# Kernel tuning notes

Hardware: AMD Instinct MI355X
Metric: run time of the kernel (lower is better)

## Reference

```python
import jax, jax.numpy as jnp
import numpy as np

DN = ('NCHW', 'OIHW', 'NCHW')


def conv2d(x, w, b, stride):
    y = jax.lax.conv_general_dilated(x, w, (stride, stride), 'VALID', dimension_numbers=DN)
    return y + b[None, :, None, None]


def split_heads(t, heads):
    # 'B (c h) H W -> B h (H W) c'  (channel index = c*heads + h)
    B, C, H, W = t.shape
    c = C // heads
    t = t.reshape(B, c, heads, H * W)
    return jnp.transpose(t, (0, 2, 3, 1))  # [B, h, HW, c]


def setup_inputs() -> dict:
    key = jax.random.key(0)
    ks = jax.random.split(key, 7)
    B, dim, H, W = 4, 256, 128, 128
    inner, p = 256, 8
    s = 0.02
    return {
        'x':  jax.random.normal(ks[0], (B, dim, H, W), jnp.float32),
        'Wq': jax.random.normal(ks[1], (inner, dim, 1, 1), jnp.float32) * s,
        'bq': jax.random.normal(ks[2], (inner,), jnp.float32) * s,
        'Wk': jax.random.normal(ks[3], (inner, dim, p, p), jnp.float32) * s,
        'bk': jax.random.normal(ks[4], (inner,), jnp.float32) * s,
        'Wv': jax.random.normal(ks[5], (inner, dim, p, p), jnp.float32) * s,
        'bv': jax.random.normal(ks[6], (inner,), jnp.float32) * s,
    }


def reference(x, Wq, bq, Wk, bk, Wv, bv):
    heads = 8
    p = Wk.shape[-1]
    B, C, H, W = x.shape
    q = conv2d(x, Wq, bq, 1)      # [B, inner, H, W]
    k = conv2d(x, Wk, bk, p)      # [B, inner, H/p, W/p]
    v = conv2d(x, Wv, bv, p)
    q = split_heads(q, heads)     # [B, h, HW, c]
    k = split_heads(k, heads)     # [B, h, K, c]
    v = split_heads(v, heads)
    # NOTE: original module applies no 1/sqrt(d) scaling
    dots = jnp.einsum('bhnc,bhkc->bhnk', q, k)
    attn = jax.nn.softmax(dots, axis=-1)
    out = jnp.einsum('bhnk,bhkc->bhnc', attn, v)  # [B, h, HW, c]
    # 'B h (H W) c -> B (c h) H W'
    c = out.shape[-1]
    out = jnp.transpose(out, (0, 3, 1, 2)).reshape(B, c * heads, H, W)
    return out
```

## Files before the change

### kernel.cpp

```cpp
#include <hip/hip_runtime.h>
#include <stdint.h>

typedef short sh4 __attribute__((ext_vector_type(4)));
typedef short short8 __attribute__((ext_vector_type(8)));
typedef float f32x4 __attribute__((ext_vector_type(4)));
typedef _Float16 half4 __attribute__((ext_vector_type(4)));
typedef _Float16 half8 __attribute__((ext_vector_type(8)));
typedef unsigned int uint2v __attribute__((ext_vector_type(2)));

__device__ __forceinline__ short f2h(float f) {
    _Float16 h = (_Float16)f;
    return __builtin_bit_cast(short, h);
}

__device__ __forceinline__ f32x4 mfma_k32(short8 a, short8 b, f32x4 c) {
    return __builtin_amdgcn_mfma_f32_16x16x32_f16(
        __builtin_bit_cast(half8, a), __builtin_bit_cast(half8, b), c, 0, 0, 0);
}
__device__ __forceinline__ f32x4 mfma_k16(half4 a, half4 b, f32x4 c) {
    return __builtin_amdgcn_mfma_f32_16x16x16f16(a, b, c, 0, 0, 0);
}
__device__ __forceinline__ unsigned int pkrtz(float a, float b) {
    return __builtin_bit_cast(unsigned int, __builtin_amdgcn_cvt_pkrtz(a, b));
}
__device__ __forceinline__ float exp2_raw(float x) {
    float r;
    asm("v_exp_f32 %0, %1" : "=v"(r) : "v"(x));
    return r;
}


__device__ __forceinline__ void transpose64(const float* __restrict__ src,
                                            short* __restrict__ dst,
                                            int srcSlowStride, int dstRowStride) {
    __shared__ float tile[64][65];
    const int t = threadIdx.x;
#pragma unroll
    for (int i = 0; i < 16; ++i) {
        int idx = i * 256 + t;
        int fast = idx & 63, slow = idx >> 6;
        tile[slow][fast] = src[(long)slow * srcSlowStride + fast];
    }
    __syncthreads();
#pragma unroll
    for (int i = 0; i < 2; ++i) {
        int ch = i * 256 + t;
        int fast = ch >> 3, sg = ch & 7;
        short8 v;
#pragma unroll
        for (int j = 0; j < 8; ++j) v[j] = f2h(tile[sg * 8 + j][fast]);
        *(short8*)(dst + (long)fast * dstRowStride + sg * 8) = v;
    }
}

__global__ __launch_bounds__(256) void k_pack_x(const float* __restrict__ x,
                                                short* __restrict__ xn) {
    int bi = blockIdx.x;
    int ct = bi & 3, pxt = (bi >> 2) & 255, b = bi >> 10;
    const float* src = x + (((long)(b * 256 + ct * 64)) << 14) + (long)pxt * 64;
    short* dst = xn + (((long)(b << 14) + pxt * 64) * 256) + ct * 64;
    transpose64(src, dst, 16384, 256);
}

__global__ __launch_bounds__(256) void k_pack_w(const float* __restrict__ wk,
                                                const float* __restrict__ wv,
                                                short* __restrict__ wp) {
    int bi = blockIdx.x;
    int ct = bi & 3, oc = bi >> 2;
    const float* base = (oc < 256) ? (wk + (long)oc * 16384) : (wv + (long)(oc - 256) * 16384);
    const float* src = base + ct * 4096;
    short* dst = wp + (long)oc * 16384 + ct * 64;
    transpose64(src, dst, 64, 256);
}

__global__ __launch_bounds__(256) void k_pack_wq(const float* __restrict__ wq,
                                                 short* __restrict__ wqp) {
    int i = blockIdx.x * 256 + threadIdx.x;
    wqp[i] = f2h(wq[i]);
}

__global__ __launch_bounds__(256) void k_kv_gemm(const short* __restrict__ xn,
                                                 const short* __restrict__ wp,
                                                 float* __restrict__ part) {
    __shared__ short Al[128 * 64];
    __shared__ short Bl[64 * 64];
    int bid = blockIdx.x;
    int wg = (bid & 7) * 64 + (bid >> 3);
    int nb = wg & 7, pm = (wg >> 3) & 7, kc = wg >> 6;
    int t = threadIdx.x, l = t & 63, w = t >> 6;
    int wm = w >> 1, wn = w & 1;
    int low = l & 15, q = l >> 4;

    short* lda[4];
    short* ldb[2];
#pragma unroll
    for (int i = 0; i < 4; ++i) {
        int g = i * 256 + t;
        int row = g >> 3, lg = g & 7;
        lda[i] = Al + row * 64 + ((lg ^ (row & 7)) * 8);
    }
#pragma unroll
    for (int i = 0; i < 2; ++i) {
        int g = i * 256 + t;
        int row = g >> 3, lg = g & 7;
        ldb[i] = Bl + row * 64 + ((lg ^ (row & 7)) * 8);
    }

    f32x4 acc[4][2];
#pragma unroll
    for (int mt = 0; mt < 4; ++mt)
#pragma unroll
        for (int nt = 0; nt < 2; ++nt) acc[mt][nt] = (f32x4){0.f, 0.f, 0.f, 0.f};

#pragma unroll 1
    for (int kk4 = 0; kk4 < 8; ++kk4) {
        const short* apt[4];
        const short* bpt[2];
        int dydx = kc * 8 + kk4;
#pragma unroll
        for (int i = 0; i < 4; ++i) {
            int g = i * 256 + t;
            int row = g >> 3, lg = g & 7;
            int patch = pm * 128 + row;
            int bb = patch >> 8, pid = patch & 255;
            int ph = pid >> 4, pw = pid & 15;
            int px = (ph * 8 + (dydx >> 3)) * 128 + pw * 8 + (dydx & 7);
            apt[i] = xn + ((long)(bb << 14) + px) * 256 + lg * 8;
        }
#pragma unroll
        for (int i = 0; i < 2; ++i) {
            int g = i * 256 + t;
            int row = g >> 3, lg = g & 7;
            int oc = nb * 64 + row;
            bpt[i] = wp + (long)oc * 16384 + kc * 2048 + kk4 * 256 + lg * 8;
        }
#pragma unroll
        for (int j = 0; j < 4; ++j) {
            short8 va[4], vb[2];
#pragma unroll
            for (int i = 0; i < 4; ++i) va[i] = *(const short8*)(apt[i] + j * 64);
#pragma unroll
            for (int i = 0; i < 2; ++i) vb[i] = *(const short8*)(bpt[i] + j * 64);
#pragma unroll
            for (int i = 0; i < 4; ++i) *(short8*)lda[i] = va[i];
#pragma unroll
            for (int i = 0; i < 2; ++i) *(short8*)ldb[i] = vb[i];
            __syncthreads();
#pragma unroll
            for (int ks = 0; ks < 2; ++ks) {
                short8 af[4], bf[2];
#pragma unroll
                for (int mt = 0; mt < 4; ++mt) {
                    int row = wm * 64 + mt * 16 + low;
                    int lg = ks * 4 + q;
                    af[mt] = *(const short8*)(Al + row * 64 + ((lg ^ (row & 7)) * 8));
                }
#pragma unroll
                for (int nt = 0; nt < 2; ++nt) {
                    int row = wn * 32 + nt * 16 + low;
                    int lg = ks * 4 + q;
                    bf[nt] = *(const short8*)(Bl + row * 64 + ((lg ^ (row & 7)) * 8));
                }
#pragma unroll
                for (int mt = 0; mt < 4; ++mt)
#pragma unroll
                    for (int nt = 0; nt < 2; ++nt)
                        acc[mt][nt] = mfma_k32(af[mt], bf[nt], acc[mt][nt]);
            }
            __syncthreads();
        }
    }
#pragma unroll
    for (int mt = 0; mt < 4; ++mt) {
        int patch = pm * 128 + wm * 64 + mt * 16 + q * 4;
#pragma unroll
        for (int nt = 0; nt < 2; ++nt) {
            int oc = nb * 64 + wn * 32 + nt * 16 + low;
#pragma unroll
            for (int r = 0; r < 4; ++r)
                part[((long)kc * 1024 + patch + r) * 512 + oc] = acc[mt][nt][r];
        }
    }
}

__global__ __launch_bounds__(256) void k_kv_fin(const float* __restrict__ part,
                                                const float* __restrict__ bk,
                                                const float* __restrict__ bv,
                                                short* __restrict__ kp,
                                                short* __restrict__ vp) {
    int idx = blockIdx.x * 256 + threadIdx.x;
    int oc = idx & 511, patch = idx >> 9;
    float s = 0.f;
#pragma unroll
    for (int kc = 0; kc < 8; ++kc) s += part[(long)kc * 524288 + idx];
    int b = patch >> 8, key = patch & 255;
    if (oc < 256) {
        s += bk[oc];
        kp[(((long)(b * 8 + (oc & 7)) * 256) + key) * 32 + (oc >> 3)] = f2h(s);
    } else {
        int o = oc - 256;
        s += bv[o];
        vp[(((long)(b * 8 + (o & 7)) * 32) + (o >> 3)) * 256 + key] = f2h(s);
    }
}

__global__ __launch_bounds__(256) void k_q_gemm(const short* __restrict__ xn,
                                                const short* __restrict__ wqp,
                                                const float* __restrict__ bq,
                                                short* __restrict__ qp) {
    __shared__ short Tb[64 * 256];
    int bi = blockIdx.x;
    int b = bi >> 8, tile = bi & 255;
    long px0 = (long)tile * 64;
    int t = threadIdx.x, l = t & 63, w = t >> 6;
    int low = l & 15, q = l >> 4;

    const short* xb = xn + (((long)(b << 14)) + px0) * 256;

    float bqv[4];
#pragma unroll
    for (int nt = 0; nt < 4; ++nt) bqv[nt] = bq[w * 64 + nt * 16 + low];

    f32x4 acc[4][4];
#pragma unroll
    for (int mt = 0; mt < 4; ++mt)
#pragma unroll
        for (int nt = 0; nt < 4; ++nt) acc[mt][nt] = (f32x4){0.f, 0.f, 0.f, 0.f};

#pragma unroll
    for (int kstep = 0; kstep < 8; ++kstep) {
        short8 af[4], bf[4];
#pragma unroll
        for (int mt = 0; mt < 4; ++mt)
            af[mt] = *(const short8*)(xb + (mt * 16 + low) * 256 + kstep * 32 + q * 8);
#pragma unroll
        for (int nt = 0; nt < 4; ++nt)
            bf[nt] = *(const short8*)(wqp + (w * 64 + nt * 16 + low) * 256 + kstep * 32 + q * 8);
#pragma unroll
        for (int mt = 0; mt < 4; ++mt)
#pragma unroll
            for (int nt = 0; nt < 4; ++nt)
                acc[mt][nt] = mfma_k32(af[mt], bf[nt], acc[mt][nt]);
    }
    const float LOG2E = 1.44269504088896f;
#pragma unroll
    for (int mt = 0; mt < 4; ++mt)
#pragma unroll
        for (int nt = 0; nt < 4; ++nt) {
            int oc = w * 64 + nt * 16 + low;
            int h8 = oc & 7, cc = oc >> 3;
            int gi = h8 * 4 + (cc >> 3);
#pragma unroll
            for (int r = 0; r < 4; ++r) {
                int px = mt * 16 + q * 4 + r;
                Tb[px * 256 + ((gi ^ (px & 7)) * 8) + (cc & 7)] =
                    f2h((acc[mt][nt][r] + bqv[nt]) * LOG2E);
            }
        }
    __syncthreads();
#pragma unroll
    for (int i = 0; i < 8; ++i) {
        int g = i * 256 + t;
        int pxl = g >> 5, g16 = g & 31;
        int hh = g16 >> 2, oct = g16 & 3;
        short8 v = *(const short8*)(Tb + pxl * 256 + ((g16 ^ (pxl & 7)) * 8));
        *(short8*)(qp + (((long)(b * 8 + hh) * 16384) + px0 + pxl) * 32 + oct * 8) = v;
    }
}

__global__ __launch_bounds__(256) void k_attn(const short* __restrict__ qp,
                                              const short* __restrict__ kp,
                                              const short* __restrict__ vp,
                                              float* __restrict__ out) {
    __shared__ short Vl[32 * 264];
    int bi = blockIdx.x;
    int tile = bi & 63, h = (bi >> 6) & 7, b = bi >> 9;
    int bh = b * 8 + h;
    long px0 = (long)tile * 256;
    int t = threadIdx.x, l = t & 63, w = t >> 6;
    int low = l & 15, q = l >> 4;

    const short* kbase = kp + (long)bh * 8192;
    const short* vbase = vp + (long)bh * 8192;
    const short* qbase = qp + (long)bh * 16384 * 32;

#pragma unroll
    for (int i = 0; i < 4; ++i) {
        int g = i * 256 + t;
        int c = g >> 5, k8 = g & 31;
        *(short8*)(Vl + c * 264 + k8 * 8) = *(const short8*)(vbase + c * 256 + k8 * 8);
    }
    short8 kf[16];
#pragma unroll
    for (int mt = 0; mt < 16; ++mt)
        kf[mt] = *(const short8*)(kbase + (mt * 16 + low) * 32 + q * 8);
    __syncthreads();

    const short* vA = Vl + low * 264 + q * 4;
    const sh4 sone = {0x3C00, 0x3C00, 0x3C00, 0x3C00};
    const half4 vones = __builtin_bit_cast(half4, sone);

#pragma unroll 1
    for (int nt = 0; nt < 4; ++nt) {
        long px = px0 + w * 64 + nt * 16 + low;
        short8 bq2 = *(const short8*)(qbase + px * 32 + q * 8);

        f32x4 dd[16];
        float m = -1e30f;
#pragma unroll
        for (int mt = 0; mt < 16; ++mt) {
            dd[mt] = mfma_k32(kf[mt], bq2, (f32x4){0.f, 0.f, 0.f, 0.f});
            m = fmaxf(fmaxf(dd[mt][0], dd[mt][1]), m);
            m = fmaxf(fmaxf(dd[mt][2], dd[mt][3]), m);
        }
        m = fmaxf(m, __shfl_xor(m, 16));
        m = fmaxf(m, __shfl_xor(m, 32));

        uint2v pk[16];
#pragma unroll
        for (int mt = 0; mt < 16; ++mt) {
            float p0 = exp2_raw(dd[mt][0] - m);
            float p1 = exp2_raw(dd[mt][1] - m);
            float p2 = exp2_raw(dd[mt][2] - m);
            float p3 = exp2_raw(dd[mt][3] - m);
            pk[mt][0] = pkrtz(p0, p1);
            pk[mt][1] = pkrtz(p2, p3);
        }

        f32x4 o2[2], os;
        o2[0] = (f32x4){0.f, 0.f, 0.f, 0.f};
        o2[1] = (f32x4){0.f, 0.f, 0.f, 0.f};
        os    = (f32x4){0.f, 0.f, 0.f, 0.f};
        __builtin_amdgcn_s_setprio(1);
#pragma unroll
        for (int kc = 0; kc < 16; ++kc) {
            half4 pb = __builtin_bit_cast(half4, pk[kc]);
            half4 av0 = __builtin_bit_cast(half4, *(const sh4*)(vA + kc * 16));
            half4 av1 = __builtin_bit_cast(half4, *(const sh4*)(vA + 4224 + kc * 16));
            o2[0] = mfma_k16(av0, pb, o2[0]);
            o2[1] = mfma_k16(av1, pb, o2[1]);
            os    = mfma_k16(vones, pb, os);
        }
        __builtin_amdgcn_s_setprio(0);
        float inv = 1.0f / os[0];

#pragma unroll
        for (int ct = 0; ct < 2; ++ct)
#pragma unroll
            for (int r = 0; r < 4; ++r) {
                int c = ct * 16 + q * 4 + r;
                out[(((long)(b * 256 + c * 8 + h)) << 14) + px] = o2[ct][r] * inv;
            }
    }
}

extern "C" void kernel_launch(void* const* d_in, const int* in_sizes, int n_in,
                              void* d_out, int out_size, void* d_ws, size_t ws_size,
                              hipStream_t stream) {
    const float* x  = (const float*)d_in[0];
    const float* Wq = (const float*)d_in[1];
    const float* bq = (const float*)d_in[2];
    const float* Wk = (const float*)d_in[3];
    const float* bk = (const float*)d_in[4];
    const float* Wv = (const float*)d_in[5];
    const float* bv = (const float*)d_in[6];
    float* out = (float*)d_out;

    char* ws = (char*)d_ws;
    const size_t OFF_XN = 0;
    const size_t OFF_Q  = 33554432;
    const size_t OFF_WP = 67108864;
    const size_t OFF_WQ = 83886080;
    const size_t OFF_KP = 84017152;
    const size_t OFF_VP = 84541440;
    const size_t OFF_PT = 85065728;
    const size_t NEEDED = 118620160;
    if (ws_size < NEEDED) return;

    short* xn  = (short*)(ws + OFF_XN);
    short* qp  = (short*)(ws + OFF_Q);
    short* wp  = (short*)(ws + OFF_WP);
    short* wqp = (short*)(ws + OFF_WQ);
    short* kp  = (short*)(ws + OFF_KP);
    short* vp  = (short*)(ws + OFF_VP);
    float* part= (float*)(ws + OFF_PT);

    k_pack_x <<<dim3(4096), dim3(256), 0, stream>>>(x, xn);
    k_pack_w <<<dim3(2048), dim3(256), 0, stream>>>(Wk, Wv, wp);
    k_pack_wq<<<dim3(256),  dim3(256), 0, stream>>>(Wq, wqp);
    k_kv_gemm<<<dim3(512),  dim3(256), 0, stream>>>(xn, wp, part);
    k_kv_fin <<<dim3(2048), dim3(256), 0, stream>>>(part, bk, bv, kp, vp);
    k_q_gemm <<<dim3(1024), dim3(256), 0, stream>>>(xn, wqp, bq, qp);
    k_attn   <<<dim3(2048), dim3(256), 0, stream>>>(qp, kp, vp, out);
}
```

Measured before the change: 143.0 us.

## Drop LDS staging in KV conv GEMM and load MFMA fragments directly from global

After: 226.9 us. +58.7%, slower.

```diff
diff --git a/kernel.cpp b/kernel.cpp
--- a/kernel.cpp
+++ b/kernel.cpp
@@ -4,6 +4,7 @@
 typedef short sh4 __attribute__((ext_vector_type(4)));
 typedef short short8 __attribute__((ext_vector_type(8)));
 typedef float f32x4 __attribute__((ext_vector_type(4)));
+typedef float f4 __attribute__((ext_vector_type(4)));
 typedef _Float16 half4 __attribute__((ext_vector_type(4)));
 typedef _Float16 half8 __attribute__((ext_vector_type(8)));
 typedef unsigned int uint2v __attribute__((ext_vector_type(2)));
@@ -36,10 +37,14 @@
     __shared__ float tile[64][65];
     const int t = threadIdx.x;
 #pragma unroll
-    for (int i = 0; i < 16; ++i) {
-        int idx = i * 256 + t;
+    for (int i = 0; i < 4; ++i) {
+        int idx = i * 1024 + t * 4;
         int fast = idx & 63, slow = idx >> 6;
-        tile[slow][fast] = src[(long)slow * srcSlowStride + fast];
+        f4 v = *(const f4*)(src + (long)slow * srcSlowStride + fast);
+        tile[slow][fast]     = v[0];
+        tile[slow][fast + 1] = v[1];
+        tile[slow][fast + 2] = v[2];
+        tile[slow][fast + 3] = v[3];
     }
     __syncthreads();
 #pragma unroll
@@ -82,97 +87,54 @@
 __global__ __launch_bounds__(256) void k_kv_gemm(const short* __restrict__ xn,
                                                  const short* __restrict__ wp,
                                                  float* __restrict__ part) {
-    __shared__ short Al[128 * 64];
-    __shared__ short Bl[64 * 64];
     int bid = blockIdx.x;
-    int wg = (bid & 7) * 64 + (bid >> 3);
-    int nb = wg & 7, pm = (wg >> 3) & 7, kc = wg >> 6;
+    int wg = (bid & 7) * 128 + (bid >> 3);
+    int nb = wg & 7, pm = (wg >> 3) & 15, kc = wg >> 7;
     int t = threadIdx.x, l = t & 63, w = t >> 6;
     int wm = w >> 1, wn = w & 1;
     int low = l & 15, q = l >> 4;
 
-    short* lda[4];
-    short* ldb[2];
-#pragma unroll
-    for (int i = 0; i < 4; ++i) {
-        int g = i * 256 + t;
-        int row = g >> 3, lg = g & 7;
-        lda[i] = Al + row * 64 + ((lg ^ (row & 7)) * 8);
-    }
-#pragma unroll
-    for (int i = 0; i < 2; ++i) {
-        int g = i * 256 + t;
-        int row = g >> 3, lg = g & 7;
-        ldb[i] = Bl + row * 64 + ((lg ^ (row & 7)) * 8);
-    }
-
-    f32x4 acc[4][2];
-#pragma unroll
-    for (int mt = 0; mt < 4; ++mt)
+    f32x4 acc[2][2];
+#pragma unroll
+    for (int mt = 0; mt < 2; ++mt)
 #pragma unroll
         for (int nt = 0; nt < 2; ++nt) acc[mt][nt] = (f32x4){0.f, 0.f, 0.f, 0.f};
+
+    const short* bbase[2];
+#pragma unroll
+    for (int nt = 0; nt < 2; ++nt)
+        bbase[nt] = wp + (long)(nb * 64 + wn * 32 + nt * 16 + low) * 16384
+                       + kc * 2048 + q * 8;
 
 #pragma unroll 1
     for (int kk4 = 0; kk4 < 8; ++kk4) {
-        const short* apt[4];
-        const short* bpt[2];
         int dydx = kc * 8 + kk4;
-#pragma unroll
-        for (int i = 0; i < 4; ++i) {
-            int g = i * 256 + t;
-            int row = g >> 3, lg = g & 7;
-            int patch = pm * 128 + row;
+        const short* apt[2];
+#pragma unroll
+        for (int mt = 0; mt < 2; ++mt) {
+            int patch = pm * 64 + wm * 32 + mt * 16 + low;
             int bb = patch >> 8, pid = patch & 255;
             int ph = pid >> 4, pw = pid & 15;
             int px = (ph * 8 + (dydx >> 3)) * 128 + pw * 8 + (dydx & 7);
-            apt[i] = xn + ((long)(bb << 14) + px) * 256 + lg * 8;
-        }
-#pragma unroll
-        for (int i = 0; i < 2; ++i) {
-            int g = i * 256 + t;
-            int row = g >> 3, lg = g & 7;
-            int oc = nb * 64 + row;
-            bpt[i] = wp + (long)oc * 16384 + kc * 2048 + kk4 * 256 + lg * 8;
-        }
-#pragma unroll
-        for (int j = 0; j < 4; ++j) {
-            short8 va[4], vb[2];
-#pragma unroll
-            for (int i = 0; i < 4; ++i) va[i] = *(const short8*)(apt[i] + j * 64);
-#pragma unroll
-            for (int i = 0; i < 2; ++i) vb[i] = *(const short8*)(bpt[i] + j * 64);
-#pragma unroll
-            for (int i = 0; i < 4; ++i) *(short8*)lda[i] = va[i];
-#pragma unroll
-            for (int i = 0; i < 2; ++i) *(short8*)ldb[i] = vb[i];
-            __syncthreads();
-#pragma unroll
-            for (int ks = 0; ks < 2; ++ks) {
-                short8 af[4], bf[2];
-#pragma unroll
-                for (int mt = 0; mt < 4; ++mt) {
-                    int row = wm * 64 + mt * 16 + low;
-                    int lg = ks * 4 + q;
-                    af[mt] = *(const short8*)(Al + row * 64 + ((lg ^ (row & 7)) * 8));
-                }
-#pragma unroll
-                for (int nt = 0; nt < 2; ++nt) {
-                    int row = wn * 32 + nt * 16 + low;
-                    int lg = ks * 4 + q;
-                    bf[nt] = *(const short8*)(Bl + row * 64 + ((lg ^ (row & 7)) * 8));
-                }
-#pragma unroll
-                for (int mt = 0; mt < 4; ++mt)
-#pragma unroll
-                    for (int nt = 0; nt < 2; ++nt)
-                        acc[mt][nt] = mfma_k32(af[mt], bf[nt], acc[mt][nt]);
-            }
-            __syncthreads();
-        }
-    }
-#pragma unroll
-    for (int mt = 0; mt < 4; ++mt) {
-        int patch = pm * 128 + wm * 64 + mt * 16 + q * 4;
+            apt[mt] = xn + ((long)(bb << 14) + px) * 256 + q * 8;
+        }
+        const short* bpt0 = bbase[0] + kk4 * 256;
+        const short* bpt1 = bbase[1] + kk4 * 256;
+#pragma unroll
+        for (int jk = 0; jk < 8; ++jk) {
+            short8 a0 = *(const short8*)(apt[0] + jk * 32);
+            short8 a1 = *(const short8*)(apt[1] + jk * 32);
+            short8 b0 = *(const short8*)(bpt0 + jk * 32);
+            short8 b1 = *(const short8*)(bpt1 + jk * 32);
+            acc[0][0] = mfma_k32(a0, b0, acc[0][0]);
+            acc[0][1] = mfma_k32(a0, b1, acc[0][1]);
+            acc[1][0] = mfma_k32(a1, b0, acc[1][0]);
+            acc[1][1] = mfma_k32(a1, b1, acc[1][1]);
+        }
+    }
+#pragma unroll
+    for (int mt = 0; mt < 2; ++mt) {
+        int patch = pm * 64 + wm * 32 + mt * 16 + q * 4;
 #pragma unroll
         for (int nt = 0; nt < 2; ++nt) {
             int oc = nb * 64 + wn * 32 + nt * 16 + low;
@@ -388,7 +350,7 @@
     k_pack_x <<<dim3(4096), dim3(256), 0, stream>>>(x, xn);
     k_pack_w <<<dim3(2048), dim3(256), 0, stream>>>(Wk, Wv, wp);
     k_pack_wq<<<dim3(256),  dim3(256), 0, stream>>>(Wq, wqp);
-    k_kv_gemm<<<dim3(512),  dim3(256), 0, stream>>>(xn, wp, part);
+    k_kv_gemm<<<dim3(1024), dim3(256), 0, stream>>>(xn, wp, part);
     k_kv_fin <<<dim3(2048), dim3(256), 0, stream>>>(part, bk, bv, kp, vp);
     k_q_gemm <<<dim3(1024), dim3(256), 0, stream>>>(xn, wqp, bq, qp);
     k_attn   <<<dim3(2048), dim3(256), 0, stream>>>(qp, kp, vp, out);
```
